# Kernel tuning notes

Measured on AMD Instinct MI355X. Metric: run time of the kernel, lower is better.

## Reference

```python
import jax, jax.numpy as jnp
import numpy as np

N, E, IN_DIM, OUT_DIM, H = 50000, 800000, 128, 16, 8


def setup_inputs() -> dict:
    key = jax.random.key(0)
    ks = jax.random.split(key, 10)
    h = jax.random.normal(ks[0], (N, IN_DIM), dtype=jnp.float32)
    row = jnp.sort(jax.random.randint(ks[1], (E,), 0, N))
    col = jax.random.randint(ks[2], (E,), 0, N)
    s = 1.0 / np.sqrt(IN_DIM)
    Wq = jax.random.normal(ks[3], (IN_DIM, OUT_DIM * H), dtype=jnp.float32) * s
    Wk = jax.random.normal(ks[4], (IN_DIM, OUT_DIM * H), dtype=jnp.float32) * s
    Wv = jax.random.normal(ks[5], (IN_DIM, OUT_DIM * H), dtype=jnp.float32) * s
    bq = jnp.zeros((OUT_DIM * H,), jnp.float32)
    bk = jnp.zeros((OUT_DIM * H,), jnp.float32)
    bv = jnp.zeros((OUT_DIM * H,), jnp.float32)
    return {"h": h, "Wq": Wq, "bq": bq, "Wk": Wk, "bk": bk, "Wv": Wv, "bv": bv,
            "row": row, "col": col}


def reference(h, Wq, bq, Wk, bk, Wv, bv, row, col):
    n = h.shape[0]
    scaling = OUT_DIM ** (-0.5)
    # projections, reshaped (N, out_dim, heads) as in the torch module
    q = (h @ Wq + bq).reshape(n, OUT_DIM, H) * scaling
    k = (h @ Wk + bk).reshape(n, OUT_DIM, H)
    v = (h @ Wv + bv).reshape(n, OUT_DIM, H)
    # bsddmm: per-edge, per-head dot product  score[e,h] = <q[row[e],:,h], k[col[e],:,h]>
    s = jnp.einsum('edh,edh->eh', q[row], k[col])  # [E, H]
    # sparse row-wise softmax (over each destination node's neighbors)
    m = jax.ops.segment_max(s, row, num_segments=n)       # [N, H]
    p = jnp.exp(s - m[row])                               # [E, H]
    z = jax.ops.segment_sum(p, row, num_segments=n)       # [N, H]
    attn = p / z[row]                                     # [E, H]
    # bspmm: out[i,d,h] = sum_{e: row[e]=i} attn[e,h] * v[col[e],d,h]
    out = jax.ops.segment_sum(attn[:, None, :] * v[col], row, num_segments=n)
    return out.reshape(n, -1)
```

## Files before the change

kernel.cpp:

```cpp
#include <hip/hip_runtime.h>
#include <math.h>

typedef unsigned int uint32;
typedef _Float16 f16x8 __attribute__((ext_vector_type(8)));
typedef _Float16 f16x2 __attribute__((ext_vector_type(2)));
typedef float f32x4 __attribute__((ext_vector_type(4)));

union frag_u { f16x8 h; uint32 u[4]; uint4 q; };


__device__ __forceinline__ uint32 pack_f16(float lo, float hi) {
    auto r = __builtin_amdgcn_cvt_pkrtz(lo, hi);
    return __builtin_bit_cast(uint32, r);
}
__device__ __forceinline__ float dot2acc(uint32 a, uint32 b, float c) {
#if __has_builtin(__builtin_amdgcn_fdot2)
    return __builtin_amdgcn_fdot2(__builtin_bit_cast(f16x2, a),
                                  __builtin_bit_cast(f16x2, b), c, false);
#else
    f16x2 av = __builtin_bit_cast(f16x2, a), bv = __builtin_bit_cast(f16x2, b);
    return fmaf((float)av[0], (float)bv[0], fmaf((float)av[1], (float)bv[1], c));
#endif
}

__global__ __launch_bounds__(256) void prep_kernel(
    const float* __restrict__ Wq, const float* __restrict__ Wk,
    const float* __restrict__ Wv, uint32* __restrict__ Wt)
{
    const int t = threadIdx.x;
    __shared__ unsigned short tile[128][129];
    const int m = blockIdx.x;
    const float* W = (m == 0) ? Wq : (m == 1) ? Wk : Wv;
    const float4* W4 = reinterpret_cast<const float4*>(W);
    #pragma unroll
    for (int i0 = 0; i0 < 16; ++i0) {
        int i = t + i0 * 256;
        int k = i >> 5, nq = i & 31;
        float4 v = W4[i];
        tile[nq * 4 + 0][k] = (unsigned short)(pack_f16(v.x, 0.f) & 0xFFFFu);
        tile[nq * 4 + 1][k] = (unsigned short)(pack_f16(v.y, 0.f) & 0xFFFFu);
        tile[nq * 4 + 2][k] = (unsigned short)(pack_f16(v.z, 0.f) & 0xFFFFu);
        tile[nq * 4 + 3][k] = (unsigned short)(pack_f16(v.w, 0.f) & 0xFFFFu);
    }
    __syncthreads();
    uint32* out = Wt + (size_t)m * 8192;
    #pragma unroll
    for (int i0 = 0; i0 < 32; ++i0) {
        int i = t + i0 * 256;
        int n = i >> 6, kp = i & 63;
        out[i] = (uint32)tile[n][kp * 2] | ((uint32)tile[n][kp * 2 + 1] << 16);
    }
}

__global__ __launch_bounds__(256) void proj_mfma_kernel(
    const float* __restrict__ h, const uint32* __restrict__ Wt,
    const float* __restrict__ bq, const float* __restrict__ bk,
    const float* __restrict__ bv,
    uint32* __restrict__ Qp, uint2* __restrict__ KV,
    const int* __restrict__ row, int* __restrict__ rp,
    int N, int E, int PB)
{
    const int t = threadIdx.x;
    if ((int)blockIdx.x >= PB) {
        int i = ((int)blockIdx.x - PB) * 256 + t;
        if (i > N) return;
        int lo = 0, hi = E;
        while (lo < hi) {
            int mid = (lo + hi) >> 1;
            if (row[mid] < i) lo = mid + 1; else hi = mid;
        }
        rp[i] = lo;
        return;
    }

    const int lane = t & 63;
    const int w = t >> 6;
    const int r = lane & 15, g = lane >> 4;
    const int rbase = blockIdx.x * 128 + w * 32;

    frag_u afr[2][4];
    const float4* h4 = reinterpret_cast<const float4*>(h);
    #pragma unroll
    for (int ng = 0; ng < 2; ++ng) {
        int arow = rbase + ng * 16 + r;
        bool av = arow < N;
        #pragma unroll
        for (int kb = 0; kb < 4; ++kb) {
            float4 x = make_float4(0.f,0.f,0.f,0.f), y = x;
            if (av) {
                size_t base = (size_t)arow * 32 + (kb * 4 + g) * 2;
                x = h4[base]; y = h4[base + 1];
            }
            afr[ng][kb].u[0] = pack_f16(x.x, x.y);
            afr[ng][kb].u[1] = pack_f16(x.z, x.w);
            afr[ng][kb].u[2] = pack_f16(y.x, y.y);
            afr[ng][kb].u[3] = pack_f16(y.z, y.w);
        }
    }

    const float SCALE_Q = 0.25f * 1.44269504f;

    #pragma unroll
    for (int tp = 0; tp < 4; ++tp) {
        const int c = tp * 16 + r;
        uint32 kpk[2][4];
        #pragma unroll
        for (int mat = 0; mat < 3; ++mat) {
            const uint32* wb = Wt + mat * 8192;
            frag_u bfr[2][4];
            #pragma unroll
            for (int tti = 0; tti < 2; ++tti)
                #pragma unroll
                for (int kb = 0; kb < 4; ++kb)
                    bfr[tti][kb].q = *reinterpret_cast<const uint4*>(
                        wb + ((tp + 4 * tti) * 16 + r) * 64 + (kb * 4 + g) * 4);

            f32x4 acc[2][2];
            #pragma unroll
            for (int ng = 0; ng < 2; ++ng)
                #pragma unroll
                for (int tti = 0; tti < 2; ++tti)
                    acc[ng][tti] = (f32x4){0.f, 0.f, 0.f, 0.f};

            #pragma unroll
            for (int ng = 0; ng < 2; ++ng)
                #pragma unroll
                for (int tti = 0; tti < 2; ++tti)
                    #pragma unroll
                    for (int kb = 0; kb < 4; ++kb)
                        acc[ng][tti] = __builtin_amdgcn_mfma_f32_16x16x32_f16(
                            afr[ng][kb].h, bfr[tti][kb].h, acc[ng][tti], 0, 0, 0);

            const float* bias = (mat == 0) ? bq : (mat == 1) ? bk : bv;
            float blo = bias[c], bhi = bias[c + 64];
            #pragma unroll
            for (int ng = 0; ng < 2; ++ng) {
                #pragma unroll
                for (int reg = 0; reg < 4; ++reg) {
                    int node = rbase + ng * 16 + g * 4 + reg;
                    float lo = acc[ng][0][reg] + blo;
                    float hi = acc[ng][1][reg] + bhi;
                    if (mat == 0) {
                        if (node < N)
                            Qp[(size_t)node * 64 + c] = pack_f16(lo * SCALE_Q, hi * SCALE_Q);
                    } else if (mat == 1) {
                        kpk[ng][reg] = pack_f16(lo, hi);
                    } else {
                        if (node < N)
                            KV[(size_t)node * 64 + c] = make_uint2(kpk[ng][reg], pack_f16(lo, hi));
                    }
                }
            }
        }
    }
}

__global__ __launch_bounds__(128) void edge_attn_kernel(
    const uint32* __restrict__ Qp, const uint2* __restrict__ KV,
    const int* __restrict__ rp, const int* __restrict__ col,
    float* __restrict__ out, int N)
{
    const int lane = threadIdx.x & 63;
    const int node = blockIdx.x * 2 + (threadIdx.x >> 6);
    if (node >= N) return;
    const int hh   = lane & 7;
    const int slot = lane >> 3;

    const int start = rp[node], end = rp[node + 1];
    float* outp = out + (size_t)node * 128;
    if (start >= end) { outp[lane] = 0.f; outp[lane + 64] = 0.f; return; }
    const int last = end - 1;

    uint32 q[8];
    {
        const uint32* qrow = Qp + (size_t)node * 64;
        #pragma unroll
        for (int i = 0; i < 8; ++i) q[i] = qrow[hh + 8 * i];
    }

    float z = 0.f;
    float acc[16];
    #pragma unroll
    for (int i = 0; i < 16; ++i) acc[i] = 0.f;

    uint2 bufA[8], bufB[8];
    #define LOADG(buf, c0) { \
        const uint2* kvr = KV + (size_t)(c0) * 64; \
        _Pragma("unroll") \
        for (int i = 0; i < 8; ++i) (buf)[i] = kvr[hh + 8 * i]; }
    #define PROC(buf, gb) { \
        float s = 0.f; \
        _Pragma("unroll") \
        for (int i = 0; i < 8; ++i) s = dot2acc(q[i], (buf)[i].x, s); \
        float p = ((gb) + slot < end) ? __builtin_amdgcn_exp2f(s) : 0.f; \
        z += p; \
        _Pragma("unroll") \
        for (int i = 0; i < 8; ++i) { \
            f16x2 hv = __builtin_bit_cast(f16x2, (buf)[i].y); \
            acc[i]     = fmaf(p, (float)hv[0], acc[i]); \
            acc[8 + i] = fmaf(p, (float)hv[1], acc[8 + i]); } }

    int cA = col[min(start + slot, last)];
    int cB = col[min(start + 8 + slot, last)];
    LOADG(bufA, cA);
    int gb = start;
    while (true) {
        LOADG(bufB, cB);
        cA = col[min(gb + 16 + slot, last)];
        PROC(bufA, gb);
        gb += 8;
        if (gb >= end) break;
        LOADG(bufA, cA);
        cB = col[min(gb + 16 + slot, last)];
        PROC(bufB, gb);
        gb += 8;
        if (gb >= end) break;
    }

    #pragma unroll
    for (int m = 8; m <= 32; m <<= 1) {
        z += __shfl_xor(z, m);
        #pragma unroll
        for (int i = 0; i < 16; ++i) acc[i] += __shfl_xor(acc[i], m);
    }

    const float rz = 1.0f / z;
    outp[lane]      = acc[slot] * rz;
    outp[lane + 64] = acc[8 + slot] * rz;
}

extern "C" void kernel_launch(void* const* d_in, const int* in_sizes, int n_in,
                              void* d_out, int out_size, void* d_ws, size_t ws_size,
                              hipStream_t stream)
{
    const float* h  = (const float*)d_in[0];
    const float* Wq = (const float*)d_in[1];
    const float* bq = (const float*)d_in[2];
    const float* Wk = (const float*)d_in[3];
    const float* bk = (const float*)d_in[4];
    const float* Wv = (const float*)d_in[5];
    const float* bv = (const float*)d_in[6];
    const int* row  = (const int*)d_in[7];
    const int* col  = (const int*)d_in[8];
    float* out = (float*)d_out;

    const int N = in_sizes[0] / 128;
    const int E = in_sizes[7];

    uint2*  KV = (uint2*)d_ws;
    uint32* Qp = (uint32*)(KV + (size_t)N * 64);
    uint32* Wt = Qp + (size_t)N * 64;
    int*    rp = (int*)(Wt + 3 * 8192);

    const int PB = (N + 127) / 128;
    const int rp_blocks = (N + 1 + 255) / 256;

    prep_kernel<<<3, 256, 0, stream>>>(Wq, Wk, Wv, Wt);
    proj_mfma_kernel<<<PB + rp_blocks, 256, 0, stream>>>(
        h, Wt, bq, bk, bv, Qp, KV, row, rp, N, E, PB);
    edge_attn_kernel<<<(N + 1) / 2, 128, 0, stream>>>(Qp, KV, rp, col, out, N);
}
```

Before: 102.1 us.

## Fuse weight transpose into projection kernel via swizzled shared-memory staging

Removes the separate weight-preparation kernel. Each projection block now loads Wq/Wk/Wv from global memory, converts them to fp16, and stores them transposed into a 32KB XOR-swizzled shared-memory tile before reading B fragments for the MFMA. The loop order becomes matrix-outer, so K results for all four tiles are kept in registers until V is computed. This saves one kernel launch and a global round trip, but every one of the roughly 391 blocks now redoes the weight conversion, adds barriers and shared-memory use, and may lose occupancy.

Measured after the change: 89.92 us (median of 2 runs). 1.14x faster.

```diff
diff --git a/kernel.cpp b/kernel.cpp
--- a/kernel.cpp
+++ b/kernel.cpp
@@ -23,37 +23,10 @@
 #endif
 }
 
-__global__ __launch_bounds__(256) void prep_kernel(
+__global__ __launch_bounds__(256) void proj_mfma_kernel(
+    const float* __restrict__ h,
     const float* __restrict__ Wq, const float* __restrict__ Wk,
-    const float* __restrict__ Wv, uint32* __restrict__ Wt)
-{
-    const int t = threadIdx.x;
-    __shared__ unsigned short tile[128][129];
-    const int m = blockIdx.x;
-    const float* W = (m == 0) ? Wq : (m == 1) ? Wk : Wv;
-    const float4* W4 = reinterpret_cast<const float4*>(W);
-    #pragma unroll
-    for (int i0 = 0; i0 < 16; ++i0) {
-        int i = t + i0 * 256;
-        int k = i >> 5, nq = i & 31;
-        float4 v = W4[i];
-        tile[nq * 4 + 0][k] = (unsigned short)(pack_f16(v.x, 0.f) & 0xFFFFu);
-        tile[nq * 4 + 1][k] = (unsigned short)(pack_f16(v.y, 0.f) & 0xFFFFu);
-        tile[nq * 4 + 2][k] = (unsigned short)(pack_f16(v.z, 0.f) & 0xFFFFu);
-        tile[nq * 4 + 3][k] = (unsigned short)(pack_f16(v.w, 0.f) & 0xFFFFu);
-    }
-    __syncthreads();
-    uint32* out = Wt + (size_t)m * 8192;
-    #pragma unroll
-    for (int i0 = 0; i0 < 32; ++i0) {
-        int i = t + i0 * 256;
-        int n = i >> 6, kp = i & 63;
-        out[i] = (uint32)tile[n][kp * 2] | ((uint32)tile[n][kp * 2 + 1] << 16);
-    }
-}
-
-__global__ __launch_bounds__(256) void proj_mfma_kernel(
-    const float* __restrict__ h, const uint32* __restrict__ Wt,
+    const float* __restrict__ Wv,
     const float* __restrict__ bq, const float* __restrict__ bk,
     const float* __restrict__ bv,
     uint32* __restrict__ Qp, uint2* __restrict__ KV,
@@ -73,6 +46,8 @@
         return;
     }
 
+    __shared__ uint32 Wl[8192];
+
     const int lane = t & 63;
     const int w = t >> 6;
     const int r = lane & 15, g = lane >> 4;
@@ -99,21 +74,48 @@
     }
 
     const float SCALE_Q = 0.25f * 1.44269504f;
-
-    #pragma unroll
-    for (int tp = 0; tp < 4; ++tp) {
-        const int c = tp * 16 + r;
-        uint32 kpk[2][4];
-        #pragma unroll
-        for (int mat = 0; mat < 3; ++mat) {
-            const uint32* wb = Wt + mat * 8192;
+    uint32 kpk[4][2][4];
+
+    #pragma unroll
+    for (int mat = 0; mat < 3; ++mat) {
+        const float* W = (mat == 0) ? Wq : (mat == 1) ? Wk : Wv;
+        const float* bias = (mat == 0) ? bq : (mat == 1) ? bk : bv;
+
+        __syncthreads();
+        {
+            const float4* W4 = reinterpret_cast<const float4*>(W);
+            #pragma unroll
+            for (int i0 = 0; i0 < 8; ++i0) {
+                int i = t + i0 * 256;
+                int k2 = i >> 5, nq = i & 31;
+                float4 a = W4[(k2 * 2) * 32 + nq];
+                float4 b = W4[(k2 * 2 + 1) * 32 + nq];
+                int slot = k2 >> 2, rem = k2 & 3;
+                #pragma unroll
+                for (int e = 0; e < 4; ++e) {
+                    int n = nq * 4 + e;
+                    float lo = (e == 0) ? a.x : (e == 1) ? a.y : (e == 2) ? a.z : a.w;
+                    float hi = (e == 0) ? b.x : (e == 1) ? b.y : (e == 2) ? b.z : b.w;
+                    Wl[n * 64 + ((slot ^ (n & 7)) << 2) + rem] = pack_f16(lo, hi);
+                }
+            }
+        }
+        __syncthreads();
+
+        #pragma unroll
+        for (int tp = 0; tp < 4; ++tp) {
+            const int c = tp * 16 + r;
+
             frag_u bfr[2][4];
             #pragma unroll
             for (int tti = 0; tti < 2; ++tti)
                 #pragma unroll
-                for (int kb = 0; kb < 4; ++kb)
+                for (int kb = 0; kb < 4; ++kb) {
+                    int n = (tp + 4 * tti) * 16 + r;
+                    int s = kb * 4 + g;
                     bfr[tti][kb].q = *reinterpret_cast<const uint4*>(
-                        wb + ((tp + 4 * tti) * 16 + r) * 64 + (kb * 4 + g) * 4);
+                        &Wl[n * 64 + ((s ^ (n & 7)) << 2)]);
+                }
 
             f32x4 acc[2][2];
             #pragma unroll
@@ -131,7 +133,6 @@
                         acc[ng][tti] = __builtin_amdgcn_mfma_f32_16x16x32_f16(
                             afr[ng][kb].h, bfr[tti][kb].h, acc[ng][tti], 0, 0, 0);
 
-            const float* bias = (mat == 0) ? bq : (mat == 1) ? bk : bv;
             float blo = bias[c], bhi = bias[c + 64];
             #pragma unroll
             for (int ng = 0; ng < 2; ++ng) {
@@ -144,10 +145,11 @@
                         if (node < N)
                             Qp[(size_t)node * 64 + c] = pack_f16(lo * SCALE_Q, hi * SCALE_Q);
                     } else if (mat == 1) {
-                        kpk[ng][reg] = pack_f16(lo, hi);
+                        kpk[tp][ng][reg] = pack_f16(lo, hi);
                     } else {
                         if (node < N)
-                            KV[(size_t)node * 64 + c] = make_uint2(kpk[ng][reg], pack_f16(lo, hi));
+                            KV[(size_t)node * 64 + c] =
+                                make_uint2(kpk[tp][ng][reg], pack_f16(lo, hi));
                     }
                 }
             }
@@ -249,14 +251,12 @@
 
     uint2*  KV = (uint2*)d_ws;
     uint32* Qp = (uint32*)(KV + (size_t)N * 64);
-    uint32* Wt = Qp + (size_t)N * 64;
-    int*    rp = (int*)(Wt + 3 * 8192);
+    int*    rp = (int*)(Qp + (size_t)N * 64);
 
     const int PB = (N + 127) / 128;
     const int rp_blocks = (N + 1 + 255) / 256;
 
-    prep_kernel<<<3, 256, 0, stream>>>(Wq, Wk, Wv, Wt);
     proj_mfma_kernel<<<PB + rp_blocks, 256, 0, stream>>>(
-        h, Wt, bq, bk, bv, Qp, KV, row, rp, N, E, PB);
+        h, Wq, Wk, Wv, bq, bk, bv, Qp, KV, row, rp, N, E, PB);
     edge_attn_kernel<<<(N + 1) / 2, 128, 0, stream>>>(Qp, KV, rp, col, out, N);
 }
```
